# Kernel optimization log

Measured on AMD Instinct MI355X. Metric: run time of the kernel, lower is better.

## Reference

```python
import jax, jax.numpy as jnp
import numpy as np

B, S, H, D = 2, 2048, 16, 64
DIM = H * D          # 1024, fused QKV dense outputs 3*DIM
EPS = 1e-6
NINF = -10000.0      # additive mask value from module
STD = 0.02           # truncated-normal init stddev (plain normal here)


def setup_inputs() -> dict:
    key = jax.random.key(0)
    k0, k1, k2 = jax.random.split(key, 3)
    x = jax.random.normal(k0, (B, S, DIM), jnp.float32)
    ln_g = jnp.ones((DIM,), jnp.float32)
    ln_b = jnp.zeros((DIM,), jnp.float32)
    wqkv = jax.random.normal(k1, (DIM, 3 * DIM), jnp.float32) * STD
    bqkv = jnp.zeros((3 * DIM,), jnp.float32)
    wo = jax.random.normal(k2, (DIM, DIM), jnp.float32) * STD
    bo = jnp.zeros((DIM,), jnp.float32)
    return {"x": x, "ln_g": ln_g, "ln_b": ln_b, "wqkv": wqkv,
            "bqkv": bqkv, "wo": wo, "bo": bo}


def reference(x, ln_g, ln_b, wqkv, bqkv, wo, bo):
    b, s, _ = x.shape
    # pre-norm LayerNorm (axis=-1, eps=1e-6)
    mu = jnp.mean(x, axis=-1, keepdims=True)
    var = jnp.mean(jnp.square(x - mu), axis=-1, keepdims=True)
    h = (x - mu) * jax.lax.rsqrt(var + EPS) * ln_g + ln_b
    # fused QKV projection, split along feature axis
    qkv = h @ wqkv + bqkv                       # [b, s, 3*DIM]
    q, k, v = jnp.split(qkv, 3, axis=2)

    def heads(t):                               # [b, s, DIM] -> [b, H, s, D]
        return t.reshape(b, s, H, D).transpose(0, 2, 1, 3)

    q, k, v = heads(q), heads(k), heads(v)
    scores = jnp.einsum("bhqd,bhkd->bhqk", q, k) / jnp.sqrt(jnp.float32(D))
    # causal mask: positions j > i get ninf (mask=None path, Lq == Lk)
    causal = (jnp.arange(s)[:, None] < jnp.arange(s)[None, :]).astype(jnp.float32) * NINF
    a = jax.nn.softmax(scores + causal, axis=-1)  # attdrop rate 0 -> identity
    ctx = jnp.einsum("bhqk,bhkd->bhqd", a, v)
    ctx = ctx.transpose(0, 2, 1, 3).reshape(b, s, DIM)
    # output dense + residual (drop rate 0 -> identity)
    return x + ctx @ wo + bo
```

## Files before the change

kernel.cpp:

```cpp
#include <hip/hip_runtime.h>
#include <hip/hip_bf16.h>

#define B_   2
#define S_   2048
#define H_   16
#define D_   64
#define DIM_ 1024
#define QKV_SZ (32 * 2048 * 64)

typedef __attribute__((ext_vector_type(8))) short bf16x8;
typedef __attribute__((ext_vector_type(4))) float f32x4;
typedef unsigned short u16;
typedef unsigned int u32;

static __device__ __forceinline__ u16 f2bf(float f) {
    union { float f; unsigned u; } v; v.f = f;
    unsigned u = v.u;
    unsigned r = (u + 0x7fffu + ((u >> 16) & 1u)) >> 16;
    return (u16)r;
}
static __device__ __forceinline__ float exp2_fast(float x) {
    float r; asm("v_exp_f32 %0, %1" : "=v"(r) : "v"(x)); return r;
}
static __device__ __forceinline__ u32 cvtpk_bf16(float lo, float hi) {
    u32 r; asm("v_cvt_pk_bf16_f32 %0, %1, %2" : "=v"(r) : "v"(lo), "v"(hi)); return r;
}
static __device__ __forceinline__ void gload_lds16(const u16* g, u16* l) {
    __builtin_amdgcn_global_load_lds(
        (const __attribute__((address_space(1))) void*)g,
        (__attribute__((address_space(3))) void*)l, 16, 0, 0);
}

__global__ __launch_bounds__(256) void ln_kernel(
    const float* __restrict__ x, const float* __restrict__ g,
    const float* __restrict__ b, u16* __restrict__ hb)
{
    int row = blockIdx.x;
    int t = threadIdx.x;
    const float4 v = ((const float4*)(x + row * DIM_))[t];
    float s  = v.x + v.y + v.z + v.w;
    float ss = v.x*v.x + v.y*v.y + v.z*v.z + v.w*v.w;
#pragma unroll
    for (int m = 1; m < 64; m <<= 1) { s += __shfl_xor(s, m); ss += __shfl_xor(ss, m); }
    __shared__ float rs[4], rss[4];
    int wid = t >> 6, lane = t & 63;
    if (lane == 0) { rs[wid] = s; rss[wid] = ss; }
    __syncthreads();
    s  = rs[0] + rs[1] + rs[2] + rs[3];
    ss = rss[0] + rss[1] + rss[2] + rss[3];
    float mu   = s * (1.0f / DIM_);
    float var  = ss * (1.0f / DIM_) - mu * mu;
    float rstd = rsqrtf(var + 1e-6f);
    const float4 gv = ((const float4*)g)[t];
    const float4 bv = ((const float4*)b)[t];
    ushort4 ov;
    ov.x = f2bf((v.x - mu) * rstd * gv.x + bv.x);
    ov.y = f2bf((v.y - mu) * rstd * gv.y + bv.y);
    ov.z = f2bf((v.z - mu) * rstd * gv.z + bv.z);
    ov.w = f2bf((v.w - mu) * rstd * gv.w + bv.w);
    ((ushort4*)(hb + row * DIM_))[t] = ov;
}

__global__ __launch_bounds__(256) void transpose_f32_bf16(
    const float* __restrict__ src, u16* __restrict__ dst, int R, int C)
{
    __shared__ u16 T[64][65];
    int c0 = blockIdx.x * 64, r0 = blockIdx.y * 64;
    int t = threadIdx.x;
    int rl = t >> 4, cl = (t & 15) * 4;
#pragma unroll
    for (int p = 0; p < 4; p++) {
        float4 v = *(const float4*)(src + (size_t)(r0 + rl + p * 16) * C + c0 + cl);
        T[cl + 0][rl + p * 16] = f2bf(v.x);
        T[cl + 1][rl + p * 16] = f2bf(v.y);
        T[cl + 2][rl + p * 16] = f2bf(v.z);
        T[cl + 3][rl + p * 16] = f2bf(v.w);
    }
    __syncthreads();
#pragma unroll
    for (int p = 0; p < 4; p++) {
        ushort4 o;
        o.x = T[rl + p * 16][cl + 0];
        o.y = T[rl + p * 16][cl + 1];
        o.z = T[rl + p * 16][cl + 2];
        o.w = T[rl + p * 16][cl + 3];
        *(ushort4*)(dst + (size_t)(c0 + rl + p * 16) * R + r0 + cl) = o;
    }
}

__global__ __launch_bounds__(256) void qkv_gemm128(
    const u16* __restrict__ A, const u16* __restrict__ Bw,
    const float* __restrict__ bias, u16* __restrict__ qkv)
{
    __shared__ __align__(16) u16 As[128 * 32];
    __shared__ __align__(16) u16 Bs[128 * 32];
    int t = threadIdx.x;
    int bn = blockIdx.x * 128, bm = blockIdx.y * 128;
    int wid = t >> 6, lane = t & 63;
    int wm = wid >> 1, wn = wid & 1;
    int l15 = lane & 15, l4 = lane >> 4;

    f32x4 zero = {0.f, 0.f, 0.f, 0.f};
    f32x4 acc[4][4];
#pragma unroll
    for (int i = 0; i < 4; i++)
#pragma unroll
        for (int j = 0; j < 4; j++) acc[i][j] = zero;

    const u16* aSrc = A  + (size_t)(bm + wid * 32 + (lane >> 2)) * 1024 + (lane & 3) * 8;
    const u16* bSrc = Bw + (size_t)(bn + wid * 32 + (lane >> 2)) * 1024 + (lane & 3) * 8;
    char* AsB = (char*)As + wid * 2048;
    char* BsB = (char*)Bs + wid * 2048;

    for (int k0 = 0; k0 < 1024; k0 += 32) {
        gload_lds16(aSrc + k0,             (u16*)(AsB));
        gload_lds16(aSrc + k0 + 16 * 1024, (u16*)(AsB + 1024));
        gload_lds16(bSrc + k0,             (u16*)(BsB));
        gload_lds16(bSrc + k0 + 16 * 1024, (u16*)(BsB + 1024));
        __syncthreads();
        bf16x8 af[4], bf[4];
#pragma unroll
        for (int mi = 0; mi < 4; mi++)
            af[mi] = *(const bf16x8*)((char*)As + (wm * 64 + mi * 16 + l15) * 64 + l4 * 16);
#pragma unroll
        for (int ni = 0; ni < 4; ni++)
            bf[ni] = *(const bf16x8*)((char*)Bs + (wn * 64 + ni * 16 + l15) * 64 + l4 * 16);
#pragma unroll
        for (int mi = 0; mi < 4; mi++)
#pragma unroll
            for (int ni = 0; ni < 4; ni++)
                acc[mi][ni] = __builtin_amdgcn_mfma_f32_16x16x32_bf16(af[mi], bf[ni], acc[mi][ni], 0, 0, 0);
        __syncthreads();
    }
#pragma unroll
    for (int mi = 0; mi < 4; mi++)
#pragma unroll
        for (int ni = 0; ni < 4; ni++) {
            int col = bn + wn * 64 + ni * 16 + l15;
            int which = col >> 10, f = col & 1023;
            int hh = f >> 6, d = f & 63;
            float bs = bias[col];
            if (which == 2) {
                int s_base = bm + wm * 64 + mi * 16 + l4 * 4;
                int bb = s_base >> 11, s = s_base & 2047;
                ushort4 pk;
                pk.x = f2bf(acc[mi][ni][0] + bs);
                pk.y = f2bf(acc[mi][ni][1] + bs);
                pk.z = f2bf(acc[mi][ni][2] + bs);
                pk.w = f2bf(acc[mi][ni][3] + bs);
                *(ushort4*)(qkv + (size_t)2 * QKV_SZ +
                            ((size_t)(bb * 16 + hh) * 64 + d) * 2048 + s) = pk;
            } else {
                float scl = (which == 0) ? 0.18033688011112042f : 1.0f;
#pragma unroll
                for (int r = 0; r < 4; r++) {
                    int row = bm + wm * 64 + mi * 16 + l4 * 4 + r;
                    int bb = row >> 11, s = row & 2047;
                    qkv[(size_t)which * QKV_SZ + ((size_t)(bb * 16 + hh) * 2048 + s) * 64 + d] =
                        f2bf((acc[mi][ni][r] + bs) * scl);
                }
            }
        }
}

__global__ __launch_bounds__(256) void out_gemm128(
    const u16* __restrict__ A, const u16* __restrict__ Bw,
    const float* __restrict__ bias, const float* __restrict__ xres,
    float* __restrict__ out)
{
    __shared__ __align__(16) u16 As[128 * 32];
    __shared__ __align__(16) u16 Bs[128 * 32];
    int t = threadIdx.x;
    int bn = blockIdx.x * 128, bm = blockIdx.y * 128;
    int wid = t >> 6, lane = t & 63;
    int wm = wid >> 1, wn = wid & 1;
    int l15 = lane & 15, l4 = lane >> 4;

    f32x4 zero = {0.f, 0.f, 0.f, 0.f};
    f32x4 acc[4][4];
#pragma unroll
    for (int i = 0; i < 4; i++)
#pragma unroll
        for (int j = 0; j < 4; j++) acc[i][j] = zero;

    const u16* aSrc = A  + (size_t)(bm + wid * 32 + (lane >> 2)) * 1024 + (lane & 3) * 8;
    const u16* bSrc = Bw + (size_t)(bn + wid * 32 + (lane >> 2)) * 1024 + (lane & 3) * 8;
    char* AsB = (char*)As + wid * 2048;
    char* BsB = (char*)Bs + wid * 2048;

    for (int k0 = 0; k0 < 1024; k0 += 32) {
        gload_lds16(aSrc + k0,             (u16*)(AsB));
        gload_lds16(aSrc + k0 + 16 * 1024, (u16*)(AsB + 1024));
        gload_lds16(bSrc + k0,             (u16*)(BsB));
        gload_lds16(bSrc + k0 + 16 * 1024, (u16*)(BsB + 1024));
        __syncthreads();
        bf16x8 af[4], bf[4];
#pragma unroll
        for (int mi = 0; mi < 4; mi++)
            af[mi] = *(const bf16x8*)((char*)As + (wm * 64 + mi * 16 + l15) * 64 + l4 * 16);
#pragma unroll
        for (int ni = 0; ni < 4; ni++)
            bf[ni] = *(const bf16x8*)((char*)Bs + (wn * 64 + ni * 16 + l15) * 64 + l4 * 16);
#pragma unroll
        for (int mi = 0; mi < 4; mi++)
#pragma unroll
            for (int ni = 0; ni < 4; ni++)
                acc[mi][ni] = __builtin_amdgcn_mfma_f32_16x16x32_bf16(af[mi], bf[ni], acc[mi][ni], 0, 0, 0);
        __syncthreads();
    }
#pragma unroll
    for (int mi = 0; mi < 4; mi++)
#pragma unroll
        for (int ni = 0; ni < 4; ni++) {
            int col = bn + wn * 64 + ni * 16 + l15;
            float bs = bias[col];
#pragma unroll
            for (int r = 0; r < 4; r++) {
                int row = bm + wm * 64 + mi * 16 + l4 * 4 + r;
                out[(size_t)row * 1024 + col] = xres[(size_t)row * 1024 + col] + acc[mi][ni][r] + bs;
            }
        }
}

__global__ __launch_bounds__(256) void attn_kernel(
    const u16* __restrict__ qbuf, const u16* __restrict__ kbuf,
    const u16* __restrict__ vbuf, u16* __restrict__ ctx)
{
    __shared__ __align__(16) char Ks[64 * 128];
    __shared__ __align__(16) char Vt[64 * 128];
    __shared__ __align__(16) char Pb[4 * 16 * 128];

    int t = threadIdx.x, wid = t >> 6, lane = t & 63;
    int l15 = lane & 15, l4 = lane >> 4;
    int idx = blockIdx.x;
    int qt = 31 - (idx >> 5);
    int bh = idx & 31;
    int q0 = qt * 64;
    int sr = t >> 3, g = t & 7;
    int bb = bh >> 4, hh = bh & 15;
    f32x4 zero = {0.f, 0.f, 0.f, 0.f};

    const u16* Q = qbuf + (size_t)(bh * 2048 + q0 + wid * 16) * 64;
    bf16x8 aq0 = *(const bf16x8*)(Q + l15 * 64 + 8 * l4);
    bf16x8 aq1 = *(const bf16x8*)(Q + l15 * 64 + 32 + 8 * l4);

    f32x4 o[4];
#pragma unroll
    for (int f = 0; f < 4; f++) o[f] = zero;
    float m_run = -1e30f;
    float l_run = 0.f;

    int kswz = (16 * g) ^ ((sr & 7) << 4);
    char* Pw = Pb + wid * 2048;
    int prow = l15 * 128;
    int pkey = (l15 & 7) << 4;
    int qloc = wid * 16 + l15;

    const u16* Kbase = kbuf + (size_t)bh * 2048 * 64;
    const u16* Vbase = vbuf + (size_t)bh * 64 * 2048;

    bf16x8 ck0 = *(const bf16x8*)(Kbase + (size_t)sr * 64 + g * 8);
    bf16x8 ck1 = *(const bf16x8*)(Kbase + (size_t)(sr + 32) * 64 + g * 8);
    bf16x8 cv0 = *(const bf16x8*)(Vbase + (size_t)sr * 2048 + g * 8);
    bf16x8 cv1 = *(const bf16x8*)(Vbase + (size_t)(sr + 32) * 2048 + g * 8);

    for (int kt = 0; kt <= qt; ++kt) {
        *(bf16x8*)(Ks + sr * 128 + kswz) = ck0;
        *(bf16x8*)(Ks + (sr + 32) * 128 + kswz) = ck1;
        *(bf16x8*)(Vt + sr * 128 + kswz) = cv0;
        *(bf16x8*)(Vt + (sr + 32) * 128 + kswz) = cv1;
        {
            int nkt = (kt < qt) ? kt + 1 : qt;
            const u16* Kn = Kbase + (size_t)nkt * 64 * 64;
            const u16* Vn = Vbase + (size_t)nkt * 64;
            bf16x8 a = *(const bf16x8*)(Kn + (size_t)sr * 64 + g * 8);
            bf16x8 b = *(const bf16x8*)(Kn + (size_t)(sr + 32) * 64 + g * 8);
            bf16x8 c = *(const bf16x8*)(Vn + (size_t)sr * 2048 + g * 8);
            bf16x8 d = *(const bf16x8*)(Vn + (size_t)(sr + 32) * 2048 + g * 8);
            __syncthreads();

            f32x4 sc[4];
            __builtin_amdgcn_s_setprio(1);
#pragma unroll
            for (int nf = 0; nf < 4; ++nf) {
                int krow = nf * 16 + l15;
                int kkey = (krow & 7) << 4;
                bf16x8 kb0 = *(const bf16x8*)(Ks + krow * 128 + ((16 * l4) ^ kkey));
                bf16x8 kb1 = *(const bf16x8*)(Ks + krow * 128 + ((64 + 16 * l4) ^ kkey));
                f32x4 z = zero;
                z = __builtin_amdgcn_mfma_f32_16x16x32_bf16(kb0, aq0, z, 0, 0, 0);
                z = __builtin_amdgcn_mfma_f32_16x16x32_bf16(kb1, aq1, z, 0, 0, 0);
                sc[nf] = z;
            }
            __builtin_amdgcn_s_setprio(0);

            if (kt == qt) {
#pragma unroll
                for (int nf = 0; nf < 4; nf++)
#pragma unroll
                    for (int r = 0; r < 4; r++) {
                        int ka = nf * 16 + 4 * l4 + r;
                        if (ka > qloc) sc[nf][r] = -1e30f;
                    }
            }
            float lmax = sc[0][0];
#pragma unroll
            for (int nf = 0; nf < 4; nf++)
#pragma unroll
                for (int r = 0; r < 4; r++) lmax = fmaxf(lmax, sc[nf][r]);
            if (__any(lmax > m_run + 10.f)) {
                float m0 = lmax;
                m0 = fmaxf(m0, __shfl_xor(m0, 16));
                m0 = fmaxf(m0, __shfl_xor(m0, 32));
                float mn = fmaxf(m_run, m0);
                float al = exp2_fast(m_run - mn);
                l_run *= al;
                m_run = mn;
                float a0 = __shfl(al, 4 * l4 + 0);
                float a1 = __shfl(al, 4 * l4 + 1);
                float a2 = __shfl(al, 4 * l4 + 2);
                float a3 = __shfl(al, 4 * l4 + 3);
#pragma unroll
                for (int f = 0; f < 4; f++) {
                    o[f][0] *= a0; o[f][1] *= a1; o[f][2] *= a2; o[f][3] *= a3;
                }
            }
            float psum = 0.f;
#pragma unroll
            for (int nf = 0; nf < 4; nf++)
#pragma unroll
                for (int r = 0; r < 4; r++) {
                    float pv = exp2_fast(sc[nf][r] - m_run);
                    sc[nf][r] = pv; psum += pv;
                }
            l_run += psum;
#pragma unroll
            for (int nf = 0; nf < 4; nf++) {
                uint2 w;
                w.x = cvtpk_bf16(sc[nf][0], sc[nf][1]);
                w.y = cvtpk_bf16(sc[nf][2], sc[nf][3]);
                *(uint2*)(Pw + prow + ((nf * 32 + l4 * 8) ^ pkey)) = w;
            }
            __builtin_amdgcn_s_setprio(1);
#pragma unroll
            for (int kk = 0; kk < 2; kk++) {
                bf16x8 pa = *(const bf16x8*)(Pw + prow + ((64 * kk + 16 * l4) ^ pkey));
#pragma unroll
                for (int f = 0; f < 4; f++) {
                    int vrow = f * 16 + l15;
                    int vkey = (vrow & 7) << 4;
                    bf16x8 vb = *(const bf16x8*)(Vt + vrow * 128 + ((64 * kk + 16 * l4) ^ vkey));
                    o[f] = __builtin_amdgcn_mfma_f32_16x16x32_bf16(pa, vb, o[f], 0, 0, 0);
                }
            }
            __builtin_amdgcn_s_setprio(0);
            __syncthreads();
            ck0 = a; ck1 = b; cv0 = c; cv1 = d;
        }
    }
    l_run += __shfl_xor(l_run, 16);
    l_run += __shfl_xor(l_run, 32);
#pragma unroll
    for (int r = 0; r < 4; r++) {
        float lr = __shfl(l_run, 4 * l4 + r);
        float inv = 1.f / lr;
        int qa = q0 + wid * 16 + l4 * 4 + r;
        u16* dst = ctx + (size_t)(bb * 2048 + qa) * 1024 + hh * 64;
#pragma unroll
        for (int f = 0; f < 4; f++) dst[f * 16 + l15] = f2bf(o[f][r] * inv);
    }
}

extern "C" void kernel_launch(void* const* d_in, const int* in_sizes, int n_in,
                              void* d_out, int out_size, void* d_ws, size_t ws_size,
                              hipStream_t stream)
{
    const float* x    = (const float*)d_in[0];
    const float* ln_g = (const float*)d_in[1];
    const float* ln_b = (const float*)d_in[2];
    const float* wqkv = (const float*)d_in[3];
    const float* bqkv = (const float*)d_in[4];
    const float* wo   = (const float*)d_in[5];
    const float* bo   = (const float*)d_in[6];
    float* out = (float*)d_out;

    char* ws = (char*)d_ws;
    u16* hbuf  = (u16*)ws;
    u16* qkvb  = (u16*)(ws + 8388608);
    u16* ctxb  = (u16*)(ws + 33554432);
    u16* wqkvT = ctxb;
    u16* woT   = hbuf;

    transpose_f32_bf16<<<dim3(48, 16), 256, 0, stream>>>(wqkv, wqkvT, 1024, 3072);
    ln_kernel<<<4096, 256, 0, stream>>>(x, ln_g, ln_b, hbuf);
    qkv_gemm128<<<dim3(24, 32), 256, 0, stream>>>(hbuf, wqkvT, bqkv, qkvb);
    transpose_f32_bf16<<<dim3(16, 16), 256, 0, stream>>>(wo, woT, 1024, 1024);
    attn_kernel<<<1024, 256, 0, stream>>>(
        qkvb, qkvb + QKV_SZ, qkvb + 2 * QKV_SZ, ctxb);
    out_gemm128<<<dim3(8, 32), 256, 0, stream>>>(ctxb, woT, bo, x, out);
}
```

Baseline: 129.1 us.

## Double-buffer LDS tiles in QKV and output GEMMs with MFMA priority boost

Both projection GEMMs now use two LDS buffers per operand. The loads for the next K tile are issued before the MFMAs on the current tile, and the barrier count per iteration drops from two to one. s_setprio is raised around the MFMA block to favour math issue. This doubles LDS use per block to 32KB, which may reduce occupancy, and it relies on the single barrier plus the waitcnt implied by __syncthreads for correctness of the async global-to-LDS loads.

```diff
diff --git a/kernel.cpp b/kernel.cpp
--- a/kernel.cpp
+++ b/kernel.cpp
@@ -92,8 +92,8 @@
     const u16* __restrict__ A, const u16* __restrict__ Bw,
     const float* __restrict__ bias, u16* __restrict__ qkv)
 {
-    __shared__ __align__(16) u16 As[128 * 32];
-    __shared__ __align__(16) u16 Bs[128 * 32];
+    __shared__ __align__(16) u16 As[2][128 * 32];
+    __shared__ __align__(16) u16 Bs[2][128 * 32];
     int t = threadIdx.x;
     int bn = blockIdx.x * 128, bm = blockIdx.y * 128;
     int wid = t >> 6, lane = t & 63;
@@ -109,28 +109,39 @@
 
     const u16* aSrc = A  + (size_t)(bm + wid * 32 + (lane >> 2)) * 1024 + (lane & 3) * 8;
     const u16* bSrc = Bw + (size_t)(bn + wid * 32 + (lane >> 2)) * 1024 + (lane & 3) * 8;
-    char* AsB = (char*)As + wid * 2048;
-    char* BsB = (char*)Bs + wid * 2048;
-
-    for (int k0 = 0; k0 < 1024; k0 += 32) {
-        gload_lds16(aSrc + k0,             (u16*)(AsB));
-        gload_lds16(aSrc + k0 + 16 * 1024, (u16*)(AsB + 1024));
-        gload_lds16(bSrc + k0,             (u16*)(BsB));
-        gload_lds16(bSrc + k0 + 16 * 1024, (u16*)(BsB + 1024));
-        __syncthreads();
+
+#define STAGE_G(bufsel, kk) do { \
+        char* Ad = (char*)As + (bufsel) * 8192 + wid * 2048; \
+        char* Bd = (char*)Bs + (bufsel) * 8192 + wid * 2048; \
+        gload_lds16(aSrc + (kk),             (u16*)Ad); \
+        gload_lds16(aSrc + (kk) + 16 * 1024, (u16*)(Ad + 1024)); \
+        gload_lds16(bSrc + (kk),             (u16*)Bd); \
+        gload_lds16(bSrc + (kk) + 16 * 1024, (u16*)(Bd + 1024)); \
+    } while (0)
+
+    STAGE_G(0, 0);
+    __syncthreads();
+    int cur = 0;
+    for (int kt = 0; kt < 32; ++kt) {
+        if (kt < 31) STAGE_G(cur ^ 1, (kt + 1) * 32);
+        const char* Ab = (const char*)As + cur * 8192;
+        const char* Bb = (const char*)Bs + cur * 8192;
         bf16x8 af[4], bf[4];
 #pragma unroll
         for (int mi = 0; mi < 4; mi++)
-            af[mi] = *(const bf16x8*)((char*)As + (wm * 64 + mi * 16 + l15) * 64 + l4 * 16);
+            af[mi] = *(const bf16x8*)(Ab + (wm * 64 + mi * 16 + l15) * 64 + l4 * 16);
 #pragma unroll
         for (int ni = 0; ni < 4; ni++)
-            bf[ni] = *(const bf16x8*)((char*)Bs + (wn * 64 + ni * 16 + l15) * 64 + l4 * 16);
+            bf[ni] = *(const bf16x8*)(Bb + (wn * 64 + ni * 16 + l15) * 64 + l4 * 16);
+        __builtin_amdgcn_s_setprio(1);
 #pragma unroll
         for (int mi = 0; mi < 4; mi++)
 #pragma unroll
             for (int ni = 0; ni < 4; ni++)
                 acc[mi][ni] = __builtin_amdgcn_mfma_f32_16x16x32_bf16(af[mi], bf[ni], acc[mi][ni], 0, 0, 0);
+        __builtin_amdgcn_s_setprio(0);
         __syncthreads();
+        cur ^= 1;
     }
 #pragma unroll
     for (int mi = 0; mi < 4; mi++)
@@ -168,8 +179,8 @@
     const float* __restrict__ bias, const float* __restrict__ xres,
     float* __restrict__ out)
 {
-    __shared__ __align__(16) u16 As[128 * 32];
-    __shared__ __align__(16) u16 Bs[128 * 32];
+    __shared__ __align__(16) u16 As[2][128 * 32];
+    __shared__ __align__(16) u16 Bs[2][128 * 32];
     int t = threadIdx.x;
     int bn = blockIdx.x * 128, bm = blockIdx.y * 128;
     int wid = t >> 6, lane = t & 63;
@@ -185,28 +196,30 @@
 
     const u16* aSrc = A  + (size_t)(bm + wid * 32 + (lane >> 2)) * 1024 + (lane & 3) * 8;
     const u16* bSrc = Bw + (size_t)(bn + wid * 32 + (lane >> 2)) * 1024 + (lane & 3) * 8;
-    char* AsB = (char*)As + wid * 2048;
-    char* BsB = (char*)Bs + wid * 2048;
-
-    for (int k0 = 0; k0 < 1024; k0 += 32) {
-        gload_lds16(aSrc + k0,             (u16*)(AsB));
-        gload_lds16(aSrc + k0 + 16 * 1024, (u16*)(AsB + 1024));
-        gload_lds16(bSrc + k0,             (u16*)(BsB));
-        gload_lds16(bSrc + k0 + 16 * 1024, (u16*)(BsB + 1024));
-        __syncthreads();
+
+    STAGE_G(0, 0);
+    __syncthreads();
+    int cur = 0;
+    for (int kt = 0; kt < 32; ++kt) {
+        if (kt < 31) STAGE_G(cur ^ 1, (kt + 1) * 32);
+        const char* Ab = (const char*)As + cur * 8192;
+        const char* Bb = (const char*)Bs + cur * 8192;
         bf16x8 af[4], bf[4];
 #pragma unroll
         for (int mi = 0; mi < 4; mi++)
-            af[mi] = *(const bf16x8*)((char*)As + (wm * 64 + mi * 16 + l15) * 64 + l4 * 16);
+            af[mi] = *(const bf16x8*)(Ab + (wm * 64 + mi * 16 + l15) * 64 + l4 * 16);
 #pragma unroll
         for (int ni = 0; ni < 4; ni++)
-            bf[ni] = *(const bf16x8*)((char*)Bs + (wn * 64 + ni * 16 + l15) * 64 + l4 * 16);
+            bf[ni] = *(const bf16x8*)(Bb + (wn * 64 + ni * 16 + l15) * 64 + l4 * 16);
+        __builtin_amdgcn_s_setprio(1);
 #pragma unroll
         for (int mi = 0; mi < 4; mi++)
 #pragma unroll
             for (int ni = 0; ni < 4; ni++)
                 acc[mi][ni] = __builtin_amdgcn_mfma_f32_16x16x32_bf16(af[mi], bf[ni], acc[mi][ni], 0, 0, 0);
+        __builtin_amdgcn_s_setprio(0);
         __syncthreads();
+        cur ^= 1;
     }
 #pragma unroll
     for (int mi = 0; mi < 4; mi++)
```

Result: no change. 129.5 us (+0.3%).
